# Kernel tuning notes

Measured on AMD Instinct MI355X. Metric: run time of the kernel, lower is better.

## Reference

```python
import jax, jax.numpy as jnp
import numpy as np
import math

B, T1, T2, T3, D = 8, 32, 32, 16, 512
L, DL = 20, 128


def setup_inputs() -> dict:
    key = jax.random.key(0)
    ks = jax.random.split(key, 16)
    s = lambda fan: 1.0 / math.sqrt(fan)
    return {
        "f_c": jax.random.normal(ks[0], (B, T1, T2, T3, D), jnp.float32),
        "f_w": jax.random.normal(ks[1], (B, L, D), jnp.float32),
        "f_s": jax.random.normal(ks[2], (B, D), jnp.float32),
        "f_m": jax.random.normal(ks[3], (B, T1, T2, D), jnp.float32),
        "Wc_down": jax.random.normal(ks[4], (DL, D), jnp.float32) * s(D),
        "bc_down": jnp.zeros((DL,), jnp.float32),
        "Ww": jax.random.normal(ks[5], (DL, D), jnp.float32) * s(D),
        "bw": jnp.zeros((DL,), jnp.float32),
        "Ws": jax.random.normal(ks[6], (DL, D), jnp.float32) * s(D),
        "bs": jnp.zeros((DL,), jnp.float32),
        "Wq": jax.random.normal(ks[7], (DL, DL), jnp.float32) * s(DL),
        "bq": jnp.zeros((DL,), jnp.float32),
        "Wk": jax.random.normal(ks[8], (DL, DL), jnp.float32) * s(DL),
        "bk": jnp.zeros((DL,), jnp.float32),
        "Wc_up": jax.random.normal(ks[9], (D, DL), jnp.float32) * s(DL),
        "bc_up": jnp.zeros((D,), jnp.float32),
    }


def reference(f_c, f_w, f_s, f_m, Wc_down, bc_down, Ww, bw, Ws, bs,
              Wq, bq, Wk, bk, Wc_up, bc_up):
    inv_sqrt_dl = 1.0 / math.sqrt(DL)
    # 1x1 conv projections == per-position linear layers
    f_c_hat = jnp.einsum('bxyzd,ld->bxyzl', f_c, Wc_down) + bc_down  # [B,T1,T2,T3,dl]
    f_w_hat = f_w @ Ww.T + bw                                        # [B,L,dl]
    f_s_hat = f_s @ Ws.T + bs                                        # [B,dl]
    # Content attention: query from map, key/value from words
    q = f_c_hat @ Wq.T + bq                                          # [B,T1,T2,T3,dl]
    k = f_w_hat @ Wk.T + bk                                          # [B,L,dl]
    scores = jnp.einsum('bxyzd,bld->bxyzl', q, k) * inv_sqrt_dl
    attn = jax.nn.softmax(scores, axis=-1)
    f_caq = jnp.einsum('bxyzl,bld->bxyzd', attn, f_w_hat)            # [B,T1,T2,T3,dl]
    # Gate with sentence feature
    f_cq = f_c_hat * (f_caq + f_s_hat[:, None, None, None, :])
    # Self-attention over last spatial axis (T3)
    A_c = jnp.einsum('bxyzd,bxywd->bxyzw', f_cq, f_cq) * inv_sqrt_dl  # [B,T1,T2,T3,T3]
    A_c = jax.nn.softmax(A_c, axis=-1)
    f_cc_hat = jnp.einsum('bxyzw,bxywd->bxyzd', A_c, f_c_hat)
    f_cc = jnp.einsum('bxyzl,dl->bxyzd', f_cc_hat, Wc_up) + bc_up     # [B,T1,T2,T3,D]
    # Sigmoid gating residual for f_m
    g_m = jax.nn.sigmoid(f_m * f_s[:, None, None, :])
    fbar_m = g_m * f_m                                                # [B,T1,T2,D]
    return f_cc + f_c + fbar_m[:, :, :, None, :]
```

## Files before the change

kernel.cpp:

```cpp
#include <hip/hip_runtime.h>
#include <math.h>

#define B_ 8
#define T1_ 32
#define T2_ 32
#define T3_ 16
#define D_ 512
#define L_ 20
#define DL_ 128
#define M_ (B_*T1_*T2_*T3_)
#define ROWS 64

#define WS_FS   0
#define WS_SB   1024
#define WS_WDB  1184
#define WS_WUB  33952
#define WS_KQB  66720
#define WS_FWT  83104

typedef __attribute__((ext_vector_type(8))) short short8_t;
typedef __attribute__((ext_vector_type(4))) float f32x4;

__device__ __forceinline__ unsigned short f2b(float f) {
  unsigned int u = __float_as_uint(f);
  return (unsigned short)((u + 0x7fffu + ((u >> 16) & 1u)) >> 16);
}
__device__ __forceinline__ float b2f(short s) {
  return __uint_as_float(((unsigned)(unsigned short)s) << 16);
}
__device__ __forceinline__ int4 pack8(float4 a, float4 b) {
  int4 p;
  p.x = (int)f2b(a.x) | ((int)f2b(a.y) << 16);
  p.y = (int)f2b(a.z) | ((int)f2b(a.w) << 16);
  p.z = (int)f2b(b.x) | ((int)f2b(b.y) << 16);
  p.w = (int)f2b(b.z) | ((int)f2b(b.w) << 16);
  return p;
}

__global__ __launch_bounds__(256) void k0_convert(
    const float* __restrict__ Wd, const float* __restrict__ Wu,
    unsigned short* __restrict__ wdb, unsigned short* __restrict__ wub,
    unsigned short* __restrict__ kqb, unsigned short* __restrict__ fwtb) {
  int g = blockIdx.x * 256 + threadIdx.x;
  if (g < 16384) {
    float4 v = ((const float4*)Wd)[g];
    ushort4 h; h.x = f2b(v.x); h.y = f2b(v.y); h.z = f2b(v.z); h.w = f2b(v.w);
    ((ushort4*)wdb)[g] = h;
  } else {
    int q = g - 16384;
    float4 v = ((const float4*)Wu)[q];
    ushort4 h; h.x = f2b(v.x); h.y = f2b(v.y); h.z = f2b(v.z); h.w = f2b(v.w);
    ((ushort4*)wub)[q] = h;
  }
  kqb[g]  = 0;
  fwtb[g] = 0;
}

__global__ __launch_bounds__(128) void k1_small(
    const float* __restrict__ f_w, const float* __restrict__ f_s,
    const float* __restrict__ Ww, const float* __restrict__ bw,
    const float* __restrict__ Ws, const float* __restrict__ bs,
    const float* __restrict__ Wq, const float* __restrict__ bq,
    const float* __restrict__ Wk, const float* __restrict__ bk,
    unsigned short* __restrict__ kqb, unsigned short* __restrict__ fwtb,
    float* __restrict__ ws) {
  const int bl = blockIdx.x;
  const int b = bl / L_, l = bl % L_;
  const int d = threadIdx.x;
  __shared__ float s_fw[DL_];
  __shared__ float s_k[DL_];
  {
    const float* x = f_w + (size_t)(b*L_+l)*D_;
    const float* w = Ww + (size_t)d*D_;
    float acc = 0.f;
    for (int i = 0; i < D_; i += 4)
      acc += x[i]*w[i] + x[i+1]*w[i+1] + x[i+2]*w[i+2] + x[i+3]*w[i+3];
    acc += bw[d];
    s_fw[d] = acc;
    fwtb[((size_t)(b*DL_ + d))*32 + l] = f2b(acc);
  }
  if (l == 0) {
    const float* x = f_s + (size_t)b*D_;
    const float* w = Ws + (size_t)d*D_;
    float acc = 0.f;
    for (int i = 0; i < D_; i += 4)
      acc += x[i]*w[i] + x[i+1]*w[i+1] + x[i+2]*w[i+2] + x[i+3]*w[i+3];
    ws[WS_FS + b*DL_ + d] = acc + bs[d];
  }
  __syncthreads();
  {
    const float* w = Wk + (size_t)d*DL_;
    float acc = 0.f;
    for (int i = 0; i < DL_; ++i) acc += s_fw[i]*w[i];
    s_k[d] = acc + bk[d];
  }
  __syncthreads();
  {
    float acc = 0.f;
    for (int c = 0; c < DL_; ++c) acc += s_k[c] * Wq[c*DL_ + d];
    kqb[((size_t)(b*32 + l))*DL_ + d] = f2b(acc);
  }
  if (d == 0) {
    float acc = 0.f;
    for (int c = 0; c < DL_; ++c) acc += bq[c]*s_k[c];
    ws[WS_SB + b*L_ + l] = acc;
  }
}

#define SFCH_B 0
#define FCQ_B  16384
#define FC_B   FCQ_B
#define ATTN_F FCQ_B
#define R3_B   32768
#define WD_B   R3_B
#define ATB_B  R3_B
#define AC_B   (R3_B + 8192)
#define FS_B   (R3_B + 12800)
#define SB_B   (R3_B + 13312)
#define WU_B   R3_B
#define SMEM_B 49152

__global__ __launch_bounds__(512, 6) void k2_fused(
    const float* __restrict__ f_c, const unsigned short* __restrict__ wdb,
    const unsigned short* __restrict__ wub,
    const unsigned short* __restrict__ kqb, const unsigned short* __restrict__ fwtb,
    const float* __restrict__ bc_down, const float* __restrict__ bc_up,
    const float* __restrict__ f_m, const float* __restrict__ f_s,
    const float* __restrict__ ws, float* __restrict__ out) {
  __shared__ __align__(16) char smb[SMEM_B];
  float* sAttn = (float*)(smb + ATTN_F);
  float* sAc   = (float*)(smb + AC_B);
  float* sFs   = (float*)(smb + FS_B);
  float* sSb   = (float*)(smb + SB_B);

  const int t = threadIdx.x;
  const int row0 = blockIdx.x * ROWS;
  const int b = row0 >> 14;
  const int lane = t & 63, w = t >> 6;
  const int l15 = lane & 15, l4 = lane >> 4;
  const float inv_sqrt_dl = 0.08838834764831843f;
  const f32x4 z4 = {0.f, 0.f, 0.f, 0.f};

  const int sd_r  = t >> 3;
  const int sd_k8 = (t & 7) * 8;
  const int sd_swz = (sd_k8 * 2) ^ ((sd_r & 7) << 4);

  f32x4 dacc[4];
  #pragma unroll
  for (int rt = 0; rt < 4; ++rt) dacc[rt] = z4;

  {
    const int ad = w * 16 + l15;
    const int aswz = (ad & 7) << 4;
    for (int ch = 0; ch < 8; ++ch) {
      const int kc = ch * 64;
      #pragma unroll
      for (int i = 0; i < 2; ++i) {
        const int idx = t + i*512;
        const int r = idx >> 3, k8 = (idx & 7) * 8;
        *(int4*)(smb + WD_B + r*128 + ((k8*2) ^ ((r & 7) << 4))) =
          *(const int4*)(wdb + (size_t)r*D_ + kc + k8);
      }
      {
        const float* src = f_c + (size_t)(row0 + sd_r)*D_ + kc + sd_k8;
        float4 v0 = *(const float4*)src;
        float4 v1 = *(const float4*)(src + 4);
        *(int4*)(smb + FC_B + sd_r*128 + sd_swz) = pack8(v0, v1);
      }
      __syncthreads();
      #pragma unroll
      for (int ks = 0; ks < 2; ++ks) {
        short8_t afrag = *(const short8_t*)(smb + WD_B + ad*128 +
                          ((ks*64 + l4*16) ^ aswz));
        #pragma unroll
        for (int rt = 0; rt < 4; ++rt) {
          const int rr = rt*16 + l15;
          short8_t bfrag = *(const short8_t*)(smb + FC_B + rr*128 +
                            ((ks*64 + l4*16) ^ ((rr & 7) << 4)));
          dacc[rt] = __builtin_amdgcn_mfma_f32_16x16x32_bf16(afrag, bfrag, dacc[rt], 0, 0, 0);
        }
      }
      __syncthreads();
    }
  }
  {
    const int d0 = w*16 + l4*4;
    float4 bias = *(const float4*)(bc_down + d0);
    #pragma unroll
    for (int rt = 0; rt < 4; ++rt) {
      const int rr = rt*16 + l15;
      ushort4 pk;
      pk.x = f2b(dacc[rt][0] + bias.x); pk.y = f2b(dacc[rt][1] + bias.y);
      pk.z = f2b(dacc[rt][2] + bias.z); pk.w = f2b(dacc[rt][3] + bias.w);
      *(ushort4*)(smb + SFCH_B + rr*256 + ((d0*2) ^ ((rr & 7) << 4))) = pk;
    }
  }
  if (t < 32) *(float4*)(sFs + t*4) = *(const float4*)(ws + WS_FS + b*DL_ + t*4);
  if (t < L_) sSb[t] = ws[WS_SB + b*L_ + t];
  __syncthreads();

  {
    const int lt = w & 1, rt2 = w >> 1;
    const int arow = lt*16 + l15;
    const int brow = rt2*16 + l15;
    const unsigned short* kqrow = kqb + (size_t)(b*32 + arow)*DL_;
    f32x4 sacc = z4;
    #pragma unroll
    for (int ks = 0; ks < 4; ++ks) {
      short8_t af = *(const short8_t*)(kqrow + ks*32 + l4*8);
      short8_t bf = *(const short8_t*)(smb + SFCH_B + brow*256 +
                     ((ks*64 + l4*16) ^ ((brow & 7) << 4)));
      sacc = __builtin_amdgcn_mfma_f32_16x16x32_bf16(af, bf, sacc, 0, 0, 0);
    }
    const int r2 = rt2*16 + l15;
    #pragma unroll
    for (int reg = 0; reg < 4; ++reg) {
      const int lval = lt*16 + l4*4 + reg;
      if (lval < L_) sAttn[r2*21 + lval] = (sacc[reg] + sSb[lval]) * inv_sqrt_dl;
    }
  }
  __syncthreads();
  if (t < ROWS) {
    float* srow = sAttn + t*21;
    float m = -1e30f;
    for (int l = 0; l < L_; ++l) m = fmaxf(m, srow[l]);
    float sum = 0.f;
    for (int l = 0; l < L_; ++l) { float e = __expf(srow[l]-m); srow[l] = e; sum += e; }
    float inv = 1.f/sum;
    for (int l = 0; l < L_; ++l) srow[l] *= inv;
  }
  __syncthreads();
  {
    const int r = t >> 3, k8 = (t & 7) * 8;
    int4 v = {0,0,0,0};
    if (k8 < L_) {
      float vv[8];
      #pragma unroll
      for (int e = 0; e < 8; ++e) {
        const int l = k8 + e;
        vv[e] = (l < L_) ? sAttn[r*21 + l] : 0.f;
      }
      v.x = (int)f2b(vv[0]) | ((int)f2b(vv[1]) << 16);
      v.y = (int)f2b(vv[2]) | ((int)f2b(vv[3]) << 16);
      v.z = (int)f2b(vv[4]) | ((int)f2b(vv[5]) << 16);
      v.w = (int)f2b(vv[6]) | ((int)f2b(vv[7]) << 16);
    }
    *(int4*)(smb + ATB_B + r*128 + ((k8*2) ^ ((r & 7) << 4))) = v;
  }
  __syncthreads();
  {
    f32x4 cacc[4];
    #pragma unroll
    for (int rt = 0; rt < 4; ++rt) cacc[rt] = z4;
    const int arow = w*16 + l15;
    short8_t af = *(const short8_t*)(fwtb + (size_t)(b*DL_ + arow)*32 + l4*8);
    #pragma unroll
    for (int rt = 0; rt < 4; ++rt) {
      const int brow = rt*16 + l15;
      short8_t bf = *(const short8_t*)(smb + ATB_B + brow*128 +
                     ((l4*16) ^ ((brow & 7) << 4)));
      cacc[rt] = __builtin_amdgcn_mfma_f32_16x16x32_bf16(af, bf, cacc[rt], 0, 0, 0);
    }
    const int d0 = w*16 + l4*4;
    float4 fs4 = *(const float4*)(sFs + d0);
    #pragma unroll
    for (int rt = 0; rt < 4; ++rt) {
      const int r = rt*16 + l15;
      const int rs = (r & 7) << 4;
      ushort4 fh = *(const ushort4*)(smb + SFCH_B + r*256 + ((d0*2) ^ rs));
      ushort4 pk;
      pk.x = f2b(b2f((short)fh.x)*(cacc[rt][0] + fs4.x));
      pk.y = f2b(b2f((short)fh.y)*(cacc[rt][1] + fs4.y));
      pk.z = f2b(b2f((short)fh.z)*(cacc[rt][2] + fs4.z));
      pk.w = f2b(b2f((short)fh.w)*(cacc[rt][3] + fs4.w));
      *(ushort4*)(smb + FCQ_B + r*256 + ((d0*2) ^ rs)) = pk;
    }
  }
  __syncthreads();
  if (w < 4) {
    const int zrow = w*16 + l15;
    f32x4 pacc = z4;
    #pragma unroll
    for (int ks = 0; ks < 4; ++ks) {
      short8_t fq = *(const short8_t*)(smb + FCQ_B + zrow*256 +
                     ((ks*64 + l4*16) ^ ((zrow & 7) << 4)));
      pacc = __builtin_amdgcn_mfma_f32_16x16x32_bf16(fq, fq, pacc, 0, 0, 0);
    }
    float p0[4], m[4], e[4], s[4];
    #pragma unroll
    for (int reg = 0; reg < 4; ++reg) p0[reg] = pacc[reg] * inv_sqrt_dl;
    #pragma unroll
    for (int reg = 0; reg < 4; ++reg) {
      m[reg] = p0[reg];
      m[reg] = fmaxf(m[reg], __shfl_xor(m[reg], 1));
      m[reg] = fmaxf(m[reg], __shfl_xor(m[reg], 2));
      m[reg] = fmaxf(m[reg], __shfl_xor(m[reg], 4));
      m[reg] = fmaxf(m[reg], __shfl_xor(m[reg], 8));
      e[reg] = __expf(p0[reg] - m[reg]);
      s[reg] = e[reg];
      s[reg] += __shfl_xor(s[reg], 1);
      s[reg] += __shfl_xor(s[reg], 2);
      s[reg] += __shfl_xor(s[reg], 4);
      s[reg] += __shfl_xor(s[reg], 8);
    }
    #pragma unroll
    for (int reg = 0; reg < 4; ++reg)
      sAc[(w*16 + l4*4 + reg)*17 + l15] = e[reg] / s[reg];
  }
  __syncthreads();
  for (int p = t; p < ROWS*32; p += 512) {
    const int r = p >> 5, d4 = (p & 31)*4;
    const int g = r >> 4, z = r & 15;
    float ax = 0.f, ay = 0.f, az = 0.f, aw = 0.f;
    #pragma unroll
    for (int wq = 0; wq < 16; ++wq) {
      float a = sAc[(g*16+z)*17 + wq];
      const int fr = g*16 + wq;
      ushort4 fv = *(const ushort4*)(smb + SFCH_B + fr*256 + ((d4*2) ^ ((fr & 7) << 4)));
      ax += a*b2f((short)fv.x); ay += a*b2f((short)fv.y);
      az += a*b2f((short)fv.z); aw += a*b2f((short)fv.w);
    }
    ushort4 pk;
    pk.x = f2b(ax); pk.y = f2b(ay); pk.z = f2b(az); pk.w = f2b(aw);
    *(ushort4*)(smb + FCQ_B + r*256 + ((d4*2) ^ ((r & 7) << 4))) = pk;
  }
  __syncthreads();

  {
    const int su_d = t >> 4;
    const int su_k8 = (t & 15) * 8;
    const int su_swz = (su_k8 * 2) ^ ((su_d & 7) << 4);
    const int ad = (w & 3)*16 + l15;
    const int aswz = (ad & 7) << 4;
    const int rbase = (w >> 2) * 32;
    for (int ch = 0; ch < 8; ++ch) {
      {
        const unsigned short* up = wub + (size_t)ch*64*DL_ + su_k8;
        int4 u0 = *(const int4*)(up + (size_t)su_d * DL_);
        int4 u1 = *(const int4*)(up + (size_t)(su_d + 32) * DL_);
        *(int4*)(smb + WU_B + su_d * 256 + su_swz) = u0;
        *(int4*)(smb + WU_B + (su_d + 32) * 256 + su_swz) = u1;
      }
      __syncthreads();
      f32x4 uacc[2]; uacc[0] = z4; uacc[1] = z4;
      #pragma unroll
      for (int ks = 0; ks < 4; ++ks) {
        short8_t afrag = *(const short8_t*)(smb + WU_B + ad*256 +
                          ((ks*64 + l4*16) ^ aswz));
        #pragma unroll
        for (int cf = 0; cf < 2; ++cf) {
          const int rr = rbase + cf*16 + l15;
          short8_t bfrag = *(const short8_t*)(smb + FCQ_B + rr*256 +
                            ((ks*64 + l4*16) ^ ((rr & 7) << 4)));
          uacc[cf] = __builtin_amdgcn_mfma_f32_16x16x32_bf16(afrag, bfrag, uacc[cf], 0, 0, 0);
        }
      }
      {
        const int d0 = ch*64 + (w & 3)*16 + l4*4;
        float4 bias = *(const float4*)(bc_up + d0);
        float4 fs4 = *(const float4*)(f_s + (size_t)b*D_ + d0);
        #pragma unroll
        for (int cf = 0; cf < 2; ++cf) {
          const int grow = row0 + rbase + cf*16 + l15;
          const size_t obase = (size_t)grow * D_;
          float4 fm4 = *(const float4*)(f_m + ((size_t)(grow >> 4))*D_ + d0);
          float4 fc4 = *(const float4*)(f_c + obase + d0);
          float4 o;
          o.x = uacc[cf][0] + bias.x + fc4.x + fm4.x/(1.f + __expf(-fm4.x*fs4.x));
          o.y = uacc[cf][1] + bias.y + fc4.y + fm4.y/(1.f + __expf(-fm4.y*fs4.y));
          o.z = uacc[cf][2] + bias.z + fc4.z + fm4.z/(1.f + __expf(-fm4.z*fs4.z));
          o.w = uacc[cf][3] + bias.w + fc4.w + fm4.w/(1.f + __expf(-fm4.w*fs4.w));
          *(float4*)(out + obase + d0) = o;
        }
      }
      __syncthreads();
    }
  }
}

extern "C" void kernel_launch(void* const* d_in, const int* in_sizes, int n_in,
                              void* d_out, int out_size, void* d_ws, size_t ws_size,
                              hipStream_t stream) {
  (void)in_sizes; (void)n_in; (void)out_size; (void)ws_size;
  const float* f_c     = (const float*)d_in[0];
  const float* f_w     = (const float*)d_in[1];
  const float* f_s     = (const float*)d_in[2];
  const float* f_m     = (const float*)d_in[3];
  const float* Wc_down = (const float*)d_in[4];
  const float* bc_down = (const float*)d_in[5];
  const float* Ww      = (const float*)d_in[6];
  const float* bw      = (const float*)d_in[7];
  const float* Ws      = (const float*)d_in[8];
  const float* bs      = (const float*)d_in[9];
  const float* Wq      = (const float*)d_in[10];
  const float* bq      = (const float*)d_in[11];
  const float* Wk      = (const float*)d_in[12];
  const float* bk      = (const float*)d_in[13];
  const float* Wc_up   = (const float*)d_in[14];
  const float* bc_up   = (const float*)d_in[15];
  float* out = (float*)d_out;
  float* wsf = (float*)d_ws;
  unsigned short* wdb  = (unsigned short*)(wsf + WS_WDB);
  unsigned short* wub  = (unsigned short*)(wsf + WS_WUB);
  unsigned short* kqb  = (unsigned short*)(wsf + WS_KQB);
  unsigned short* fwtb = (unsigned short*)(wsf + WS_FWT);

  hipLaunchKernelGGL(k0_convert, dim3(128), dim3(256), 0, stream,
                     Wc_down, Wc_up, wdb, wub, kqb, fwtb);
  hipLaunchKernelGGL(k1_small, dim3(B_*L_), dim3(128), 0, stream,
                     f_w, f_s, Ww, bw, Ws, bs, Wq, bq, Wk, bk, kqb, fwtb, wsf);
  hipLaunchKernelGGL(k2_fused, dim3(M_/ROWS), dim3(512), 0, stream,
                     f_c, wdb, wub, kqb, fwtb, bc_down, bc_up, f_m, f_s, wsf, out);
}
```

Baseline: 243.5 us.

## Shrink LDS footprint, precompute f_m gate, use packed bf16 conversions

Repacks the shared-memory layout of the fused kernel from 48KB to about 38KB and raises launch bounds from 6 to 8 waves-per-SIMD hint, aiming for higher occupancy. The sigmoid gate on f_m moves into a separate pre-kernel that writes fbm to workspace, so the fused epilogue no longer recomputes the exp for each of the 16 T3 rows. Scalar bf16 rounding is replaced by the HIP packed float2-to-bf16 intrinsic. Adds an extra launch and an extra 16MB round trip through global memory for fbm, plus an added barrier inside the gating stage.

```diff
diff --git a/kernel.cpp b/kernel.cpp
--- a/kernel.cpp
+++ b/kernel.cpp
@@ -1,4 +1,5 @@
 #include <hip/hip_runtime.h>
+#include <hip/hip_bf16.h>
 #include <math.h>
 
 #define B_ 8
@@ -17,23 +18,31 @@
 #define WS_WUB  33952
 #define WS_KQB  66720
 #define WS_FWT  83104
+#define WS_FBM  99488
 
 typedef __attribute__((ext_vector_type(8))) short short8_t;
 typedef __attribute__((ext_vector_type(4))) float f32x4;
 
+__device__ __forceinline__ unsigned pkcvt(float a, float b) {
+  float2 v; v.x = a; v.y = b;
+  __hip_bfloat162 h = __float22bfloat162_rn(v);
+  unsigned r;
+  __builtin_memcpy(&r, &h, sizeof(r));
+  return r;
+}
 __device__ __forceinline__ unsigned short f2b(float f) {
-  unsigned int u = __float_as_uint(f);
-  return (unsigned short)((u + 0x7fffu + ((u >> 16) & 1u)) >> 16);
+  __hip_bfloat16 h = __float2bfloat16(f);
+  unsigned short r;
+  __builtin_memcpy(&r, &h, sizeof(r));
+  return r;
 }
 __device__ __forceinline__ float b2f(short s) {
   return __uint_as_float(((unsigned)(unsigned short)s) << 16);
 }
 __device__ __forceinline__ int4 pack8(float4 a, float4 b) {
   int4 p;
-  p.x = (int)f2b(a.x) | ((int)f2b(a.y) << 16);
-  p.y = (int)f2b(a.z) | ((int)f2b(a.w) << 16);
-  p.z = (int)f2b(b.x) | ((int)f2b(b.y) << 16);
-  p.w = (int)f2b(b.z) | ((int)f2b(b.w) << 16);
+  p.x = (int)pkcvt(a.x, a.y); p.y = (int)pkcvt(a.z, a.w);
+  p.z = (int)pkcvt(b.x, b.y); p.w = (int)pkcvt(b.z, b.w);
   return p;
 }
 
@@ -44,16 +53,31 @@
   int g = blockIdx.x * 256 + threadIdx.x;
   if (g < 16384) {
     float4 v = ((const float4*)Wd)[g];
-    ushort4 h; h.x = f2b(v.x); h.y = f2b(v.y); h.z = f2b(v.z); h.w = f2b(v.w);
-    ((ushort4*)wdb)[g] = h;
+    uint2 h; h.x = pkcvt(v.x, v.y); h.y = pkcvt(v.z, v.w);
+    ((uint2*)wdb)[g] = h;
   } else {
     int q = g - 16384;
     float4 v = ((const float4*)Wu)[q];
-    ushort4 h; h.x = f2b(v.x); h.y = f2b(v.y); h.z = f2b(v.z); h.w = f2b(v.w);
-    ((ushort4*)wub)[q] = h;
+    uint2 h; h.x = pkcvt(v.x, v.y); h.y = pkcvt(v.z, v.w);
+    ((uint2*)wub)[q] = h;
   }
   kqb[g]  = 0;
   fwtb[g] = 0;
+}
+
+__global__ __launch_bounds__(256) void k0b_gate(
+    const float* __restrict__ f_m, const float* __restrict__ f_s,
+    float* __restrict__ fbm) {
+  int i = blockIdx.x * 256 + threadIdx.x;
+  float4 m = ((const float4*)f_m)[i];
+  int e = i * 4; int b = e >> 19; int d0 = e & 511;
+  float4 s = *(const float4*)(f_s + (size_t)b*D_ + d0);
+  float4 g;
+  g.x = m.x/(1.f + __expf(-m.x*s.x));
+  g.y = m.y/(1.f + __expf(-m.y*s.y));
+  g.z = m.z/(1.f + __expf(-m.z*s.z));
+  g.w = m.w/(1.f + __expf(-m.w*s.w));
+  ((float4*)fbm)[i] = g;
 }
 
 __global__ __launch_bounds__(128) void k1_small(
@@ -107,25 +131,24 @@
   }
 }
 
+#define WD_B   0
 #define SFCH_B 0
+#define WU_B   0
+#define FC_B   16384
+#define ATTN_F 16384
+#define ATB_B  22528
 #define FCQ_B  16384
-#define FC_B   FCQ_B
-#define ATTN_F FCQ_B
-#define R3_B   32768
-#define WD_B   R3_B
-#define ATB_B  R3_B
-#define AC_B   (R3_B + 8192)
-#define FS_B   (R3_B + 12800)
-#define SB_B   (R3_B + 13312)
-#define WU_B   R3_B
-#define SMEM_B 49152
-
-__global__ __launch_bounds__(512, 6) void k2_fused(
+#define AC_B   32768
+#define FS_B   37120
+#define SB_B   37632
+#define SMEM_B 38912
+
+__global__ __launch_bounds__(512, 8) void k2_fused(
     const float* __restrict__ f_c, const unsigned short* __restrict__ wdb,
     const unsigned short* __restrict__ wub,
     const unsigned short* __restrict__ kqb, const unsigned short* __restrict__ fwtb,
     const float* __restrict__ bc_down, const float* __restrict__ bc_up,
-    const float* __restrict__ f_m, const float* __restrict__ f_s,
+    const float* __restrict__ fbm,
     const float* __restrict__ ws, float* __restrict__ out) {
   __shared__ __align__(16) char smb[SMEM_B];
   float* sAttn = (float*)(smb + ATTN_F);
@@ -189,10 +212,10 @@
     #pragma unroll
     for (int rt = 0; rt < 4; ++rt) {
       const int rr = rt*16 + l15;
-      ushort4 pk;
-      pk.x = f2b(dacc[rt][0] + bias.x); pk.y = f2b(dacc[rt][1] + bias.y);
-      pk.z = f2b(dacc[rt][2] + bias.z); pk.w = f2b(dacc[rt][3] + bias.w);
-      *(ushort4*)(smb + SFCH_B + rr*256 + ((d0*2) ^ ((rr & 7) << 4))) = pk;
+      uint2 pw;
+      pw.x = pkcvt(dacc[rt][0] + bias.x, dacc[rt][1] + bias.y);
+      pw.y = pkcvt(dacc[rt][2] + bias.z, dacc[rt][3] + bias.w);
+      *(uint2*)(smb + SFCH_B + rr*256 + ((d0*2) ^ ((rr & 7) << 4))) = pw;
     }
   }
   if (t < 32) *(float4*)(sFs + t*4) = *(const float4*)(ws + WS_FS + b*DL_ + t*4);
@@ -240,10 +263,10 @@
         const int l = k8 + e;
         vv[e] = (l < L_) ? sAttn[r*21 + l] : 0.f;
       }
-      v.x = (int)f2b(vv[0]) | ((int)f2b(vv[1]) << 16);
-      v.y = (int)f2b(vv[2]) | ((int)f2b(vv[3]) << 16);
-      v.z = (int)f2b(vv[4]) | ((int)f2b(vv[5]) << 16);
-      v.w = (int)f2b(vv[6]) | ((int)f2b(vv[7]) << 16);
+      v.x = (int)pkcvt(vv[0], vv[1]);
+      v.y = (int)pkcvt(vv[2], vv[3]);
+      v.z = (int)pkcvt(vv[4], vv[5]);
+      v.w = (int)pkcvt(vv[6], vv[7]);
     }
     *(int4*)(smb + ATB_B + r*128 + ((k8*2) ^ ((r & 7) << 4))) = v;
   }
@@ -254,13 +277,19 @@
     for (int rt = 0; rt < 4; ++rt) cacc[rt] = z4;
     const int arow = w*16 + l15;
     short8_t af = *(const short8_t*)(fwtb + (size_t)(b*DL_ + arow)*32 + l4*8);
-    #pragma unroll
-    for (int rt = 0; rt < 4; ++rt) {
-      const int brow = rt*16 + l15;
-      short8_t bf = *(const short8_t*)(smb + ATB_B + brow*128 +
-                     ((l4*16) ^ ((brow & 7) << 4)));
-      cacc[rt] = __builtin_amdgcn_mfma_f32_16x16x32_bf16(af, bf, cacc[rt], 0, 0, 0);
-    }
+    short8_t bf0 = *(const short8_t*)(smb + ATB_B + (0*16 + l15)*128 +
+                    ((l4*16) ^ (((0*16 + l15) & 7) << 4)));
+    short8_t bf1 = *(const short8_t*)(smb + ATB_B + (1*16 + l15)*128 +
+                    ((l4*16) ^ (((1*16 + l15) & 7) << 4)));
+    short8_t bf2 = *(const short8_t*)(smb + ATB_B + (2*16 + l15)*128 +
+                    ((l4*16) ^ (((2*16 + l15) & 7) << 4)));
+    short8_t bf3 = *(const short8_t*)(smb + ATB_B + (3*16 + l15)*128 +
+                    ((l4*16) ^ (((3*16 + l15) & 7) << 4)));
+    cacc[0] = __builtin_amdgcn_mfma_f32_16x16x32_bf16(af, bf0, cacc[0], 0, 0, 0);
+    cacc[1] = __builtin_amdgcn_mfma_f32_16x16x32_bf16(af, bf1, cacc[1], 0, 0, 0);
+    cacc[2] = __builtin_amdgcn_mfma_f32_16x16x32_bf16(af, bf2, cacc[2], 0, 0, 0);
+    cacc[3] = __builtin_amdgcn_mfma_f32_16x16x32_bf16(af, bf3, cacc[3], 0, 0, 0);
+    __syncthreads();
     const int d0 = w*16 + l4*4;
     float4 fs4 = *(const float4*)(sFs + d0);
     #pragma unroll
@@ -268,12 +297,12 @@
       const int r = rt*16 + l15;
       const int rs = (r & 7) << 4;
       ushort4 fh = *(const ushort4*)(smb + SFCH_B + r*256 + ((d0*2) ^ rs));
-      ushort4 pk;
-      pk.x = f2b(b2f((short)fh.x)*(cacc[rt][0] + fs4.x));
-      pk.y = f2b(b2f((short)fh.y)*(cacc[rt][1] + fs4.y));
-      pk.z = f2b(b2f((short)fh.z)*(cacc[rt][2] + fs4.z));
-      pk.w = f2b(b2f((short)fh.w)*(cacc[rt][3] + fs4.w));
-      *(ushort4*)(smb + FCQ_B + r*256 + ((d0*2) ^ rs)) = pk;
+      uint2 pw;
+      pw.x = pkcvt(b2f((short)fh.x)*(cacc[rt][0] + fs4.x),
+                   b2f((short)fh.y)*(cacc[rt][1] + fs4.y));
+      pw.y = pkcvt(b2f((short)fh.z)*(cacc[rt][2] + fs4.z),
+                   b2f((short)fh.w)*(cacc[rt][3] + fs4.w));
+      *(uint2*)(smb + FCQ_B + r*256 + ((d0*2) ^ rs)) = pw;
     }
   }
   __syncthreads();
@@ -320,9 +349,9 @@
       ax += a*b2f((short)fv.x); ay += a*b2f((short)fv.y);
       az += a*b2f((short)fv.z); aw += a*b2f((short)fv.w);
     }
-    ushort4 pk;
-    pk.x = f2b(ax); pk.y = f2b(ay); pk.z = f2b(az); pk.w = f2b(aw);
-    *(ushort4*)(smb + FCQ_B + r*256 + ((d4*2) ^ ((r & 7) << 4))) = pk;
+    uint2 pw;
+    pw.x = pkcvt(ax, ay); pw.y = pkcvt(az, aw);
+    *(uint2*)(smb + FCQ_B + r*256 + ((d4*2) ^ ((r & 7) << 4))) = pw;
   }
   __syncthreads();
 
@@ -358,18 +387,17 @@
       {
         const int d0 = ch*64 + (w & 3)*16 + l4*4;
         float4 bias = *(const float4*)(bc_up + d0);
-        float4 fs4 = *(const float4*)(f_s + (size_t)b*D_ + d0);
         #pragma unroll
         for (int cf = 0; cf < 2; ++cf) {
           const int grow = row0 + rbase + cf*16 + l15;
           const size_t obase = (size_t)grow * D_;
-          float4 fm4 = *(const float4*)(f_m + ((size_t)(grow >> 4))*D_ + d0);
+          float4 fb4 = *(const float4*)(fbm + ((size_t)(grow >> 4))*D_ + d0);
           float4 fc4 = *(const float4*)(f_c + obase + d0);
           float4 o;
-          o.x = uacc[cf][0] + bias.x + fc4.x + fm4.x/(1.f + __expf(-fm4.x*fs4.x));
-          o.y = uacc[cf][1] + bias.y + fc4.y + fm4.y/(1.f + __expf(-fm4.y*fs4.y));
-          o.z = uacc[cf][2] + bias.z + fc4.z + fm4.z/(1.f + __expf(-fm4.z*fs4.z));
-          o.w = uacc[cf][3] + bias.w + fc4.w + fm4.w/(1.f + __expf(-fm4.w*fs4.w));
+          o.x = uacc[cf][0] + bias.x + fc4.x + fb4.x;
+          o.y = uacc[cf][1] + bias.y + fc4.y + fb4.y;
+          o.z = uacc[cf][2] + bias.z + fc4.z + fb4.z;
+          o.w = uacc[cf][3] + bias.w + fc4.w + fb4.w;
           *(float4*)(out + obase + d0) = o;
         }
       }
@@ -404,11 +432,14 @@
   unsigned short* wub  = (unsigned short*)(wsf + WS_WUB);
   unsigned short* kqb  = (unsigned short*)(wsf + WS_KQB);
   unsigned short* fwtb = (unsigned short*)(wsf + WS_FWT);
+  float* fbm = wsf + WS_FBM;
 
   hipLaunchKernelGGL(k0_convert, dim3(128), dim3(256), 0, stream,
                      Wc_down, Wc_up, wdb, wub, kqb, fwtb);
+  hipLaunchKernelGGL(k0b_gate, dim3(4096), dim3(256), 0, stream,
+                     f_m, f_s, fbm);
   hipLaunchKernelGGL(k1_small, dim3(B_*L_), dim3(128), 0, stream,
                      f_w, f_s, Ww, bw, Ws, bs, Wq, bq, Wk, bk, kqb, fwtb, wsf);
   hipLaunchKernelGGL(k2_fused, dim3(M_/ROWS), dim3(512), 0, stream,
-                     f_c, wdb, wub, kqb, fwtb, bc_down, bc_up, f_m, f_s, wsf, out);
-}
+                     f_c, wdb, wub, kqb, fwtb, bc_down, bc_up, fbm, wsf, out);
+}
```

New measurement: 227.0 us. 1.07x faster.
